# Performance work log

Hardware: AMD Instinct MI355X
Metric: run time of the kernel (lower is better)

## Reference

```python
import jax, jax.numpy as jnp
import numpy as np

N_NODES = 100000
IN_DIM = 128
HIDDEN = 256
N_CLASSES = 16
N_EDGES = 1600000
N_GRAPHS = 64


def setup_inputs() -> dict:
    key = jax.random.key(0)
    ks = jax.random.split(key, 12)
    x = jax.random.normal(ks[0], (N_NODES, IN_DIM), dtype=jnp.float32)
    edge_index = jax.random.randint(ks[1], (2, N_EDGES), 0, N_NODES, dtype=jnp.int64)
    batch = jnp.sort(jax.random.randint(ks[2], (N_NODES,), 0, N_GRAPHS, dtype=jnp.int64))
    s = 0.05
    # SAGEConv layer 1: lin_l (on aggregated neighbors, with bias), lin_r (on root, no bias)
    W1l = jax.random.normal(ks[3], (IN_DIM, HIDDEN), dtype=jnp.float32) * s
    b1 = jnp.zeros((HIDDEN,), dtype=jnp.float32)
    W1r = jax.random.normal(ks[4], (IN_DIM, HIDDEN), dtype=jnp.float32) * s
    # SAGEConv layer 2
    W2l = jax.random.normal(ks[5], (HIDDEN, HIDDEN), dtype=jnp.float32) * s
    b2 = jnp.zeros((HIDDEN,), dtype=jnp.float32)
    W2r = jax.random.normal(ks[6], (HIDDEN, HIDDEN), dtype=jnp.float32) * s
    # final classifier
    fcW = jax.random.normal(ks[7], (HIDDEN, N_CLASSES), dtype=jnp.float32) * s
    fcb = jnp.zeros((N_CLASSES,), dtype=jnp.float32)
    return {"x": x, "edge_index": edge_index, "batch": batch,
            "W1l": W1l, "b1": b1, "W1r": W1r,
            "W2l": W2l, "b2": b2, "W2r": W2r,
            "fcW": fcW, "fcb": fcb}


def _sage_conv(x, src, dst, Wl, bl, Wr, n_nodes):
    # mean aggregation of neighbor features onto destination nodes
    agg = jax.ops.segment_sum(x[src], dst, num_segments=n_nodes)      # [N, d]
    deg = jax.ops.segment_sum(jnp.ones(src.shape, x.dtype), dst, num_segments=n_nodes)
    mean = agg / jnp.maximum(deg, 1.0)[:, None]
    # out = lin_l(mean_neighbors) + lin_r(x_root)  (PyG SAGEConv, mean aggr)
    return mean @ Wl + bl + x @ Wr


def reference(x, edge_index, batch, W1l, b1, W1r, W2l, b2, W2r, fcW, fcb):
    src, dst = edge_index[0], edge_index[1]
    h = jax.nn.relu(_sage_conv(x, src, dst, W1l, b1, W1r, N_NODES))
    # dropout is identity in inference mode
    h = jax.nn.relu(_sage_conv(h, src, dst, W2l, b2, W2r, N_NODES))
    # global mean pool over graphs in the batch
    g_sum = jax.ops.segment_sum(h, batch, num_segments=N_GRAPHS)      # [G, d]
    g_cnt = jax.ops.segment_sum(jnp.ones(batch.shape, h.dtype), batch, num_segments=N_GRAPHS)
    g = g_sum / jnp.maximum(g_cnt, 1.0)[:, None]
    return g @ fcW + fcb                                              # [G, num_classes]
```

## Files before the change

kernel.cpp:

```cpp
#include <hip/hip_runtime.h>

#define INDIM 128
#define HID 256
#define NCLS 16
#define NGRAPH 64
#define CHUNK 8192

typedef __bf16 bf16_t;
typedef bf16_t bf16x8 __attribute__((ext_vector_type(8)));
typedef float f32x4 __attribute__((ext_vector_type(4)));

__device__ __forceinline__ float bfu_lo(unsigned v) {
    union { unsigned i; float f; } u; u.i = v << 16; return u.f;
}
__device__ __forceinline__ float bfu_hi(unsigned v) {
    union { unsigned i; float f; } u; u.i = v & 0xffff0000u; return u.f;
}
__device__ __forceinline__ unsigned short f2bf(float f) {
    union { float f; unsigned i; } u; u.f = f;
    unsigned b = u.i;
    return (unsigned short)((b + 0x7fffu + ((b >> 16) & 1u)) >> 16);
}
__device__ __forceinline__ unsigned packbf(float lo, float hi) {
    return (unsigned)f2bf(lo) | ((unsigned)f2bf(hi) << 16);
}

typedef __attribute__((address_space(1))) const unsigned gu32_t;
typedef __attribute__((address_space(3))) unsigned lu32_t;
__device__ __forceinline__ void gl_lds16(const void* g, void* l) {
    __builtin_amdgcn_global_load_lds((gu32_t*)g, (lu32_t*)l, 16, 0, 0);
}

#define ACC8(a, v)                                   \
    do {                                             \
        a[0] += bfu_lo((v).x); a[1] += bfu_hi((v).x); \
        a[2] += bfu_lo((v).y); a[3] += bfu_hi((v).y); \
        a[4] += bfu_lo((v).z); a[5] += bfu_hi((v).z); \
        a[6] += bfu_lo((v).w); a[7] += bfu_hi((v).w); \
    } while (0)

__global__ void hist_kernel(const int* __restrict__ dst, int* __restrict__ deg, int E) {
    int e = blockIdx.x * blockDim.x + threadIdx.x;
    if (e < E) atomicAdd(&deg[dst[e]], 1);
}

__global__ void scan1_kernel(const int* __restrict__ deg, int* __restrict__ bsum, int n) {
    __shared__ int s[256];
    int t = threadIdx.x;
    int i = blockIdx.x * 256 + t;
    s[t] = (i < n) ? deg[i] : 0;
    __syncthreads();
    for (int off = 128; off > 0; off >>= 1) {
        if (t < off) s[t] += s[t + off];
        __syncthreads();
    }
    if (t == 0) bsum[blockIdx.x] = s[0];
}

__global__ void scan2_kernel(int* bsum, int nb) {
    __shared__ int s[1024];
    int t = threadIdx.x;
    int v = (t < nb) ? bsum[t] : 0;
    s[t] = v;
    __syncthreads();
    for (int off = 1; off < 1024; off <<= 1) {
        int u = (t >= off) ? s[t - off] : 0;
        __syncthreads();
        s[t] += u;
        __syncthreads();
    }
    if (t < nb) bsum[t] = s[t] - v;
}

__global__ void scan3_kernel(const int* __restrict__ deg, const int* __restrict__ bsum,
                             int* __restrict__ offs, int* __restrict__ gcur, int n) {
    __shared__ int s[256];
    int t = threadIdx.x;
    int i = blockIdx.x * 256 + t;
    int v = (i < n) ? deg[i] : 0;
    s[t] = v;
    __syncthreads();
    for (int off = 1; off < 256; off <<= 1) {
        int u = (t >= off) ? s[t - off] : 0;
        __syncthreads();
        s[t] += u;
        __syncthreads();
    }
    if (i < n) offs[i] = s[t] - v + bsum[blockIdx.x];
    if (t == 0) gcur[blockIdx.x] = bsum[blockIdx.x];
}

__global__ __launch_bounds__(256) void binA_kernel(const int* __restrict__ src,
                                                   const int* __restrict__ dst,
                                                   int* __restrict__ gcur,
                                                   unsigned* __restrict__ tmp,
                                                   int E, int nbuck) {
    __shared__ int hist[512];
    __shared__ int base[512];
    int t = threadIdx.x;
    int e0 = blockIdx.x * CHUNK;
    int e1 = min(e0 + CHUNK, E);
    for (int i = t; i < nbuck; i += 256) hist[i] = 0;
    __syncthreads();
    for (int e = e0 + t; e < e1; e += 256) atomicAdd(&hist[dst[e] >> 8], 1);
    __syncthreads();
    for (int i = t; i < nbuck; i += 256) {
        int c = hist[i];
        base[i] = (c > 0) ? atomicAdd(&gcur[i], c) : 0;
    }
    __syncthreads();
    for (int e = e0 + t; e < e1; e += 256) {
        int d = dst[e];
        int p = atomicAdd(&base[d >> 8], 1);
        tmp[p] = ((unsigned)(d & 255) << 17) | (unsigned)src[e];
    }
}

__global__ __launch_bounds__(256) void binB_kernel(const unsigned* __restrict__ tmp,
                                                   const int* __restrict__ offs,
                                                   int* __restrict__ srclist, int E, int n) {
    __shared__ int cur[256];
    int b = blockIdx.x;
    int node0 = b << 8;
    int nnodes = min(256, n - node0);
    int t = threadIdx.x;
    if (t < nnodes) cur[t] = offs[node0 + t];
    __syncthreads();
    int ebeg = offs[node0];
    int eend = (node0 + 256 < n) ? offs[node0 + 256] : E;
    for (int e = ebeg + t; e < eend; e += 256) {
        unsigned v = tmp[e];
        int p = atomicAdd(&cur[v >> 17], 1);
        srclist[p] = (int)(v & 0x1FFFFu);
    }
}

__global__ void prep_kernel(const float* __restrict__ x, unsigned short* __restrict__ xb,
                            const float* __restrict__ W1l, const float* __restrict__ W1r,
                            unsigned short* __restrict__ Bt1,
                            const float* __restrict__ W2l, const float* __restrict__ W2r,
                            unsigned short* __restrict__ Bt2, int castb) {
    int b = blockIdx.x, t = threadIdx.x;
    if (b < castb) {
        int i4 = (b * 256 + t) * 4;
        float4 v = *(const float4*)(x + i4);
        *(ushort4*)(xb + i4) = make_ushort4(f2bf(v.x), f2bf(v.y), f2bf(v.z), f2bf(v.w));
    } else if (b < castb + 256) {
        int idx = (b - castb) * 256 + t;
        int nn = idx >> 8, k = idx & 255;
        float v = (k < 128) ? W1l[(size_t)k * 256 + nn] : W1r[(size_t)(k - 128) * 256 + nn];
        Bt1[(size_t)nn * 256 + k] = f2bf(v);
    } else {
        int idx = (b - castb - 256) * 256 + t;
        int nn = idx >> 9, k = idx & 511;
        float v = (k < 256) ? W2l[(size_t)k * 256 + nn] : W2r[(size_t)(k - 256) * 256 + nn];
        Bt2[(size_t)nn * 512 + k] = f2bf(v);
    }
}

__global__ void agg1_kernel(const unsigned short* __restrict__ xb, const int* __restrict__ srclist,
                            const int* __restrict__ offs, const int* __restrict__ deg,
                            unsigned short* __restrict__ mean, int n) {
    int gid = blockIdx.x * blockDim.x + threadIdx.x;
    int node = gid >> 6, lane = gid & 63;
    if (node >= n) return;
    int q = lane >> 4, sub = lane & 15;
    int st = __builtin_amdgcn_readfirstlane(offs[node]);
    int d = __builtin_amdgcn_readfirstlane(deg[node]);
    int end = st + d;
    float aA[8] = {0, 0, 0, 0, 0, 0, 0, 0}, aB[8] = {0, 0, 0, 0, 0, 0, 0, 0};
    const unsigned short* rb = xb + sub * 8;
    int e = st;
    for (; e + 7 < end; e += 8) {
        int s0 = srclist[e + q];
        int s1 = srclist[e + 4 + q];
        uint4 v0 = *(const uint4*)(rb + (size_t)s0 * 128);
        uint4 v1 = *(const uint4*)(rb + (size_t)s1 * 128);
        ACC8(aA, v0);
        ACC8(aB, v1);
    }
    for (; e + 3 < end; e += 4) {
        int s0 = srclist[e + q];
        uint4 v0 = *(const uint4*)(rb + (size_t)s0 * 128);
        ACC8(aA, v0);
    }
    int rem = end - e;
    if (rem > 0) {
        int s0 = srclist[e + ((q < rem) ? q : 0)];
        uint4 v0 = *(const uint4*)(rb + (size_t)s0 * 128);
        if (q < rem) ACC8(aA, v0);
    }
    float inv = 1.f / fmaxf((float)d, 1.f);
    float tot[8];
#pragma unroll
    for (int i = 0; i < 8; ++i) {
        float s = aA[i] + aB[i];
        s += __shfl_xor(s, 16);
        s += __shfl_xor(s, 32);
        tot[i] = s * inv;
    }
    if (lane < 16) {
        uint4 o;
        o.x = packbf(tot[0], tot[1]);
        o.y = packbf(tot[2], tot[3]);
        o.z = packbf(tot[4], tot[5]);
        o.w = packbf(tot[6], tot[7]);
        *(uint4*)(mean + (size_t)node * 128 + sub * 8) = o;
    }
}

__global__ void agg2_kernel(const unsigned short* __restrict__ h1, const int* __restrict__ srclist,
                            const int* __restrict__ offs, const int* __restrict__ deg,
                            unsigned short* __restrict__ mean, int n) {
    int gid = blockIdx.x * blockDim.x + threadIdx.x;
    int node = gid >> 6, lane = gid & 63;
    if (node >= n) return;
    int half = lane >> 5, sub = lane & 31;
    int st = __builtin_amdgcn_readfirstlane(offs[node]);
    int d = __builtin_amdgcn_readfirstlane(deg[node]);
    int end = st + d;
    float aA[8] = {0, 0, 0, 0, 0, 0, 0, 0}, aB[8] = {0, 0, 0, 0, 0, 0, 0, 0};
    float aC[8] = {0, 0, 0, 0, 0, 0, 0, 0}, aD[8] = {0, 0, 0, 0, 0, 0, 0, 0};
    const unsigned short* rb = h1 + sub * 8;
    int e = st;
    for (; e + 7 < end; e += 8) {
        int s0 = srclist[e + half];
        int s1 = srclist[e + 2 + half];
        int s2 = srclist[e + 4 + half];
        int s3 = srclist[e + 6 + half];
        uint4 v0 = *(const uint4*)(rb + (size_t)s0 * 256);
        uint4 v1 = *(const uint4*)(rb + (size_t)s1 * 256);
        uint4 v2 = *(const uint4*)(rb + (size_t)s2 * 256);
        uint4 v3 = *(const uint4*)(rb + (size_t)s3 * 256);
        ACC8(aA, v0);
        ACC8(aB, v1);
        ACC8(aC, v2);
        ACC8(aD, v3);
    }
    for (; e + 1 < end; e += 2) {
        int s0 = srclist[e + half];
        uint4 v0 = *(const uint4*)(rb + (size_t)s0 * 256);
        ACC8(aA, v0);
    }
    if (e < end) {
        int s0 = srclist[e];
        uint4 v0 = *(const uint4*)(rb + (size_t)s0 * 256);
        if (half == 0) ACC8(aA, v0);
    }
    float inv = 1.f / fmaxf((float)d, 1.f);
    float tot[8];
#pragma unroll
    for (int i = 0; i < 8; ++i) {
        float s = (aA[i] + aB[i]) + (aC[i] + aD[i]);
        s += __shfl_xor(s, 32);
        tot[i] = s * inv;
    }
    if (half == 0) {
        uint4 o;
        o.x = packbf(tot[0], tot[1]);
        o.y = packbf(tot[2], tot[3]);
        o.z = packbf(tot[4], tot[5]);
        o.w = packbf(tot[6], tot[7]);
        *(uint4*)(mean + (size_t)node * 256 + sub * 8) = o;
    }
}

template <int KH>
__global__ __launch_bounds__(256) void gemm_kernel(
        const bf16_t* __restrict__ A1, const bf16_t* __restrict__ A2,
        const bf16_t* __restrict__ Bt, const float* __restrict__ bias,
        unsigned short* __restrict__ H, int M) {
    constexpr int KT = 2 * KH;
    constexpr int NC = KT / 64;
    constexpr int CPH = KH / 64;
    __shared__ unsigned short As[64 * 64];
    int t = threadIdx.x, wave = t >> 6, lane = t & 63;
    int quad = lane >> 4, l16 = lane & 15;
    int row0 = blockIdx.x * 64, n0 = wave * 64;

    f32x4 acc[4][4];
#pragma unroll
    for (int i = 0; i < 4; ++i)
#pragma unroll
        for (int j = 0; j < 4; ++j) acc[i][j] = (f32x4)(0.f);

    int rA = wave * 8 + (lane >> 3);
    int kb = lane & 7;
    int kswA = (kb ^ (rA & 7)) << 3;
    unsigned short* ldsA = &As[(size_t)(wave * 8) * 64];
    unsigned short* ldsB = &As[(size_t)(32 + wave * 8) * 64];

    const bf16_t* Bp = Bt + (size_t)(n0 + l16) * KT + quad * 8;

    for (int c = 0; c < NC; ++c) {
        const bf16_t* Ah = (c < CPH) ? A1 : A2;
        int kk = ((c < CPH) ? c : (c - CPH)) * 64;
        gl_lds16(Ah + (size_t)(row0 + rA) * KH + kk + kswA, ldsA);
        gl_lds16(Ah + (size_t)(row0 + 32 + rA) * KH + kk + kswA, ldsB);
        __syncthreads();
        int bk = c * 64;
#pragma unroll
        for (int sub = 0; sub < 2; ++sub) {
            bf16x8 af[4], bfr[4];
#pragma unroll
            for (int mi = 0; mi < 4; ++mi) {
                int r = mi * 16 + l16;
                int qb = sub * 4 + quad;
                af[mi] = *(const bf16x8*)&As[r * 64 + ((qb ^ (r & 7)) << 3)];
            }
#pragma unroll
            for (int ni = 0; ni < 4; ++ni)
                bfr[ni] = *(const bf16x8*)(Bp + (size_t)(ni * 16) * KT + bk + sub * 32);
#pragma unroll
            for (int mi = 0; mi < 4; ++mi)
#pragma unroll
                for (int ni = 0; ni < 4; ++ni)
                    acc[mi][ni] = __builtin_amdgcn_mfma_f32_16x16x32_bf16(
                        af[mi], bfr[ni], acc[mi][ni], 0, 0, 0);
        }
        __syncthreads();
    }

    float bv[4];
#pragma unroll
    for (int ni = 0; ni < 4; ++ni) bv[ni] = bias[n0 + ni * 16 + l16];
#pragma unroll
    for (int mi = 0; mi < 4; ++mi) {
#pragma unroll
        for (int r = 0; r < 4; ++r) {
            int row = row0 + mi * 16 + quad * 4 + r;
            if (row < M) {
#pragma unroll
                for (int ni = 0; ni < 4; ++ni) {
                    int col = n0 + ni * 16 + l16;
                    H[(size_t)row * 256 + col] = f2bf(fmaxf(acc[mi][ni][r] + bv[ni], 0.f));
                }
            }
        }
    }
}

__global__ void pool_kernel(const unsigned short* __restrict__ h2, const int* __restrict__ batch,
                            float* __restrict__ g, float* __restrict__ cnt, int n) {
    int col = threadIdx.x;
    int row0 = blockIdx.x * 256;
    float acc = 0.f;
    int cur = -1, seglen = 0;
    for (int r = 0; r < 256; ++r) {
        int row = row0 + r;
        if (row >= n) break;
        int b = batch[row];
        if (b != cur) {
            if (cur >= 0) {
                atomicAdd(&g[cur * 256 + col], acc);
                if (col == 0) atomicAdd(&cnt[cur], (float)seglen);
            }
            acc = 0.f; cur = b; seglen = 0;
        }
        union { unsigned i; float f; } u;
        u.i = ((unsigned)h2[(size_t)row * 256 + col]) << 16;
        acc += u.f;
        seglen++;
    }
    if (cur >= 0) {
        atomicAdd(&g[cur * 256 + col], acc);
        if (col == 0) atomicAdd(&cnt[cur], (float)seglen);
    }
}

__global__ void final_kernel(const float* __restrict__ g, const float* __restrict__ cnt,
                             const float* __restrict__ fcW, const float* __restrict__ fcb,
                             float* __restrict__ out) {
    int t = threadIdx.x;
    for (int o = t; o < NGRAPH * NCLS; o += 256) {
        int gi = o >> 4, c = o & 15;
        float inv = 1.f / fmaxf(cnt[gi], 1.f);
        float dot = 0.f;
        for (int k = 0; k < 256; ++k) dot += g[gi * 256 + k] * fcW[k * 16 + c];
        out[o] = dot * inv + fcb[c];
    }
}

extern "C" void kernel_launch(void* const* d_in, const int* in_sizes, int n_in, void* d_out,
                              int out_size, void* d_ws, size_t ws_size, hipStream_t stream) {
    const float* x   = (const float*)d_in[0];
    const int* edge  = (const int*)d_in[1];
    const int* batch = (const int*)d_in[2];
    const float* W1l = (const float*)d_in[3];
    const float* b1  = (const float*)d_in[4];
    const float* W1r = (const float*)d_in[5];
    const float* W2l = (const float*)d_in[6];
    const float* b2  = (const float*)d_in[7];
    const float* W2r = (const float*)d_in[8];
    const float* fcW = (const float*)d_in[9];
    const float* fcb = (const float*)d_in[10];
    float* out = (float*)d_out;

    const int n = in_sizes[0] / INDIM;
    const int E = in_sizes[1] / 2;
    const int* src = edge;
    const int* dst = edge + E;
    const int nbuck = (n + 255) >> 8;

    char* ws = (char*)d_ws;
    size_t off = 0;
    auto alloc = [&](size_t bytes) {
        size_t p = off;
        off = (off + bytes + 511) & ~(size_t)511;
        return p;
    };
    size_t offs_o    = alloc((size_t)n * 4);
    size_t deg_o     = alloc((size_t)n * 4);
    size_t cnt_o     = alloc(64 * 4);
    size_t g_o       = alloc(64 * 256 * 4);
    size_t zero_end  = off;
    size_t bsum_o    = alloc(1024 * 4);
    size_t gcur_o    = alloc(512 * 4);
    size_t srclist_o = alloc((size_t)E * 4);
    size_t bt1_o     = alloc(256 * 256 * 2);
    size_t bt2_o     = alloc(256 * 512 * 2);
    size_t xbm2_o    = alloc((size_t)n * 256 * 2);
    size_t mean1_o   = alloc((size_t)n * 128 * 2);
    size_t h1_o      = alloc((size_t)n * 256 * 2);
    size_t h2_o      = alloc((size_t)n * 256 * 2);

    int*   offs    = (int*)(ws + offs_o);
    int*   deg     = (int*)(ws + deg_o);
    float* cnt     = (float*)(ws + cnt_o);
    float* g       = (float*)(ws + g_o);
    int*   bsum    = (int*)(ws + bsum_o);
    int*   gcur    = (int*)(ws + gcur_o);
    int*   srclist = (int*)(ws + srclist_o);
    unsigned short* Bt1   = (unsigned short*)(ws + bt1_o);
    unsigned short* Bt2   = (unsigned short*)(ws + bt2_o);
    unsigned short* xb16  = (unsigned short*)(ws + xbm2_o);
    unsigned short* mean2 = (unsigned short*)(ws + xbm2_o);
    unsigned short* mean1 = (unsigned short*)(ws + mean1_o);
    unsigned short* h1b   = (unsigned short*)(ws + h1_o);
    unsigned*       tmp   = (unsigned*)(ws + h2_o);
    unsigned short* h2b   = (unsigned short*)(ws + h2_o);

    hipMemsetAsync(ws + deg_o, 0, zero_end - deg_o, stream);

    int eb = (E + 255) / 256;
    int nb = (n + 255) / 256;
    hist_kernel<<<eb, 256, 0, stream>>>(dst, deg, E);
    scan1_kernel<<<nb, 256, 0, stream>>>(deg, bsum, n);
    scan2_kernel<<<1, 1024, 0, stream>>>(bsum, nb);
    scan3_kernel<<<nb, 256, 0, stream>>>(deg, bsum, offs, gcur, n);
    binA_kernel<<<(E + CHUNK - 1) / CHUNK, 256, 0, stream>>>(src, dst, gcur, tmp, E, nbuck);
    binB_kernel<<<nbuck, 256, 0, stream>>>(tmp, offs, srclist, E, n);

    int castb = n * INDIM / 4 / 256;
    prep_kernel<<<castb + 256 + 512, 256, 0, stream>>>(x, xb16, W1l, W1r, Bt1, W2l, W2r, Bt2, castb);

    int aggb = (n * 64 + 255) / 256;
    int gemmb = (n + 63) / 64;

    agg1_kernel<<<aggb, 256, 0, stream>>>(xb16, srclist, offs, deg, mean1, n);
    gemm_kernel<128><<<gemmb, 256, 0, stream>>>(
        (const bf16_t*)mean1, (const bf16_t*)xb16, (const bf16_t*)Bt1, b1, h1b, n);
    agg2_kernel<<<aggb, 256, 0, stream>>>(h1b, srclist, offs, deg, mean2, n);
    gemm_kernel<256><<<gemmb, 256, 0, stream>>>(
        (const bf16_t*)mean2, (const bf16_t*)h1b, (const bf16_t*)Bt2, b2, h2b, n);

    pool_kernel<<<nb, 256, 0, stream>>>(h2b, batch, g, cnt, n);
    final_kernel<<<1, 256, 0, stream>>>(g, cnt, fcW, fcb, out);
}
```

Baseline: 641.5 us.

## Split neighbor aggregation into 64-column slices run as separate passes

```diff
diff --git a/kernel.cpp b/kernel.cpp
--- a/kernel.cpp
+++ b/kernel.cpp
@@ -158,110 +158,57 @@
     }
 }
 
-__global__ void agg1_kernel(const unsigned short* __restrict__ xb, const int* __restrict__ srclist,
+template <int STRIDE>
+__global__ void aggq_kernel(const unsigned short* __restrict__ tab,
+                            const int* __restrict__ srclist,
                             const int* __restrict__ offs, const int* __restrict__ deg,
-                            unsigned short* __restrict__ mean, int n) {
+                            unsigned short* __restrict__ mean, int n, int col0) {
     int gid = blockIdx.x * blockDim.x + threadIdx.x;
     int node = gid >> 6, lane = gid & 63;
     if (node >= n) return;
-    int q = lane >> 4, sub = lane & 15;
+    int g = lane >> 3, sub = lane & 7;
     int st = __builtin_amdgcn_readfirstlane(offs[node]);
     int d = __builtin_amdgcn_readfirstlane(deg[node]);
     int end = st + d;
     float aA[8] = {0, 0, 0, 0, 0, 0, 0, 0}, aB[8] = {0, 0, 0, 0, 0, 0, 0, 0};
-    const unsigned short* rb = xb + sub * 8;
+    const unsigned short* rb = tab + col0 + sub * 8;
     int e = st;
-    for (; e + 7 < end; e += 8) {
-        int s0 = srclist[e + q];
-        int s1 = srclist[e + 4 + q];
-        uint4 v0 = *(const uint4*)(rb + (size_t)s0 * 128);
-        uint4 v1 = *(const uint4*)(rb + (size_t)s1 * 128);
+    for (; e + 15 < end; e += 16) {
+        int s0 = srclist[e + g];
+        int s1 = srclist[e + 8 + g];
+        uint4 v0 = *(const uint4*)(rb + (size_t)s0 * STRIDE);
+        uint4 v1 = *(const uint4*)(rb + (size_t)s1 * STRIDE);
         ACC8(aA, v0);
         ACC8(aB, v1);
     }
-    for (; e + 3 < end; e += 4) {
-        int s0 = srclist[e + q];
-        uint4 v0 = *(const uint4*)(rb + (size_t)s0 * 128);
+    for (; e + 7 < end; e += 8) {
+        int s0 = srclist[e + g];
+        uint4 v0 = *(const uint4*)(rb + (size_t)s0 * STRIDE);
         ACC8(aA, v0);
     }
     int rem = end - e;
     if (rem > 0) {
-        int s0 = srclist[e + ((q < rem) ? q : 0)];
-        uint4 v0 = *(const uint4*)(rb + (size_t)s0 * 128);
-        if (q < rem) ACC8(aA, v0);
+        int s0 = srclist[e + ((g < rem) ? g : 0)];
+        uint4 v0 = *(const uint4*)(rb + (size_t)s0 * STRIDE);
+        if (g < rem) ACC8(aA, v0);
     }
     float inv = 1.f / fmaxf((float)d, 1.f);
     float tot[8];
 #pragma unroll
     for (int i = 0; i < 8; ++i) {
         float s = aA[i] + aB[i];
+        s += __shfl_xor(s, 8);
         s += __shfl_xor(s, 16);
         s += __shfl_xor(s, 32);
         tot[i] = s * inv;
     }
-    if (lane < 16) {
+    if (lane < 8) {
         uint4 o;
         o.x = packbf(tot[0], tot[1]);
         o.y = packbf(tot[2], tot[3]);
         o.z = packbf(tot[4], tot[5]);
         o.w = packbf(tot[6], tot[7]);
-        *(uint4*)(mean + (size_t)node * 128 + sub * 8) = o;
-    }
-}
-
-__global__ void agg2_kernel(const unsigned short* __restrict__ h1, const int* __restrict__ srclist,
-                            const int* __restrict__ offs, const int* __restrict__ deg,
-                            unsigned short* __restrict__ mean, int n) {
-    int gid = blockIdx.x * blockDim.x + threadIdx.x;
-    int node = gid >> 6, lane = gid & 63;
-    if (node >= n) return;
-    int half = lane >> 5, sub = lane & 31;
-    int st = __builtin_amdgcn_readfirstlane(offs[node]);
-    int d = __builtin_amdgcn_readfirstlane(deg[node]);
-    int end = st + d;
-    float aA[8] = {0, 0, 0, 0, 0, 0, 0, 0}, aB[8] = {0, 0, 0, 0, 0, 0, 0, 0};
-    float aC[8] = {0, 0, 0, 0, 0, 0, 0, 0}, aD[8] = {0, 0, 0, 0, 0, 0, 0, 0};
-    const unsigned short* rb = h1 + sub * 8;
-    int e = st;
-    for (; e + 7 < end; e += 8) {
-        int s0 = srclist[e + half];
-        int s1 = srclist[e + 2 + half];
-        int s2 = srclist[e + 4 + half];
-        int s3 = srclist[e + 6 + half];
-        uint4 v0 = *(const uint4*)(rb + (size_t)s0 * 256);
-        uint4 v1 = *(const uint4*)(rb + (size_t)s1 * 256);
-        uint4 v2 = *(const uint4*)(rb + (size_t)s2 * 256);
-        uint4 v3 = *(const uint4*)(rb + (size_t)s3 * 256);
-        ACC8(aA, v0);
-        ACC8(aB, v1);
-        ACC8(aC, v2);
-        ACC8(aD, v3);
-    }
-    for (; e + 1 < end; e += 2) {
-        int s0 = srclist[e + half];
-        uint4 v0 = *(const uint4*)(rb + (size_t)s0 * 256);
-        ACC8(aA, v0);
-    }
-    if (e < end) {
-        int s0 = srclist[e];
-        uint4 v0 = *(const uint4*)(rb + (size_t)s0 * 256);
-        if (half == 0) ACC8(aA, v0);
-    }
-    float inv = 1.f / fmaxf((float)d, 1.f);
-    float tot[8];
-#pragma unroll
-    for (int i = 0; i < 8; ++i) {
-        float s = (aA[i] + aB[i]) + (aC[i] + aD[i]);
-        s += __shfl_xor(s, 32);
-        tot[i] = s * inv;
-    }
-    if (half == 0) {
-        uint4 o;
-        o.x = packbf(tot[0], tot[1]);
-        o.y = packbf(tot[2], tot[3]);
-        o.z = packbf(tot[4], tot[5]);
-        o.w = packbf(tot[6], tot[7]);
-        *(uint4*)(mean + (size_t)node * 256 + sub * 8) = o;
+        *(uint4*)(mean + (size_t)node * STRIDE + col0 + lane * 8) = o;
     }
 }
 
@@ -457,10 +404,14 @@
     int aggb = (n * 64 + 255) / 256;
     int gemmb = (n + 63) / 64;
 
-    agg1_kernel<<<aggb, 256, 0, stream>>>(xb16, srclist, offs, deg, mean1, n);
+    aggq_kernel<128><<<aggb, 256, 0, stream>>>(xb16, srclist, offs, deg, mean1, n, 0);
+    aggq_kernel<128><<<aggb, 256, 0, stream>>>(xb16, srclist, offs, deg, mean1, n, 64);
     gemm_kernel<128><<<gemmb, 256, 0, stream>>>(
         (const bf16_t*)mean1, (const bf16_t*)xb16, (const bf16_t*)Bt1, b1, h1b, n);
-    agg2_kernel<<<aggb, 256, 0, stream>>>(h1b, srclist, offs, deg, mean2, n);
+    aggq_kernel<256><<<aggb, 256, 0, stream>>>(h1b, srclist, offs, deg, mean2, n, 0);
+    aggq_kernel<256><<<aggb, 256, 0, stream>>>(h1b, srclist, offs, deg, mean2, n, 64);
+    aggq_kernel<256><<<aggb, 256, 0, stream>>>(h1b, srclist, offs, deg, mean2, n, 128);
+    aggq_kernel<256><<<aggb, 256, 0, stream>>>(h1b, srclist, offs, deg, mean2, n, 192);
     gemm_kernel<256><<<gemmb, 256, 0, stream>>>(
         (const bf16_t*)mean2, (const bf16_t*)h1b, (const bf16_t*)Bt2, b2, h2b, n);
 
```

After: 705.3 us. 1.1x slower.
